# Performance work log

Hardware: AMD Instinct MI355X
Metric: run time of the kernel (lower is better)

## Reference

```python
import jax, jax.numpy as jnp
import numpy as np

B, T, D = 2048, 200, 64
H1, H2 = 80, 40
CONST_MIN = -4294967295.0


def setup_inputs() -> dict:
    key = jax.random.key(0)
    ks = jax.random.split(key, 10)
    q = jax.random.normal(ks[0], (B, D), dtype=jnp.float32)
    k = jax.random.normal(ks[1], (B, T, D), dtype=jnp.float32)
    v = jax.random.normal(ks[2], (B, T, D), dtype=jnp.float32)
    mask = jax.random.randint(ks[3], (B, T), 0, 2, dtype=jnp.int32)
    # MLP params: Dense(80, sigmoid) -> Dense(40, sigmoid) -> Dense(1)
    s1 = 1.0 / np.sqrt(4 * D)
    W1 = jax.random.normal(ks[4], (4 * D, H1), dtype=jnp.float32) * s1
    b1 = jnp.zeros((H1,), dtype=jnp.float32)
    W2 = jax.random.normal(ks[5], (H1, H2), dtype=jnp.float32) * (1.0 / np.sqrt(H1))
    b2 = jnp.zeros((H2,), dtype=jnp.float32)
    Wf = jax.random.normal(ks[6], (H2, 1), dtype=jnp.float32) * (1.0 / np.sqrt(H2))
    bf = jnp.zeros((1,), dtype=jnp.float32)
    return {"q": q, "k": k, "v": v, "mask": mask,
            "W1": W1, "b1": b1, "W2": W2, "b2": b2, "Wf": Wf, "bf": bf}


def reference(q, k, v, mask, W1, b1, W2, b2, Wf, bf):
    # q: [B,D] tiled over T -> [B,T,D]
    qt = jnp.broadcast_to(q[:, None, :], k.shape)
    # per-pair features [B,T,4D]
    info = jnp.concatenate([qt, k, qt - k, qt * k], axis=-1)
    h = jax.nn.sigmoid(jnp.einsum('btf,fh->bth', info, W1) + b1)
    h = jax.nn.sigmoid(jnp.einsum('bth,hg->btg', h, W2) + b2)
    logits = (jnp.einsum('btg,go->bto', h, Wf) + bf)[..., 0]  # [B,T]
    logits = jnp.where(mask == 0, jnp.float32(CONST_MIN), logits)
    w = jax.nn.softmax(logits, axis=-1)  # [B,T]
    out = jnp.einsum('bt,btd->bd', w, v)  # weighted sum of v
    return out
```

## Files before the change

### kernel.cpp

```cpp
#include <hip/hip_runtime.h>
#include <math.h>

#define T_LEN 200

typedef short bf8 __attribute__((ext_vector_type(8)));
typedef float f32x4 __attribute__((ext_vector_type(4)));

__device__ __forceinline__ float sigmoidf_(float x){ return 1.0f/(1.0f+__expf(-x)); }
__device__ __forceinline__ unsigned int pk_bf16(float lo, float hi){
  unsigned int r; asm("v_cvt_pk_bf16_f32 %0, %1, %2":"=v"(r):"v"(lo),"v"(hi)); return r;
}
__device__ __forceinline__ float bfu(short s){
  union{unsigned u; float f;} c; c.u = ((unsigned)(unsigned short)s)<<16; return c.f;
}
union U4B8 { uint4 u; bf8 b; };
__device__ __forceinline__ bf8 pack8(float4 x, float4 y){
  U4B8 r;
  r.u.x = pk_bf16(x.x,x.y); r.u.y = pk_bf16(x.z,x.w);
  r.u.z = pk_bf16(y.x,y.y); r.u.w = pk_bf16(y.z,y.w);
  return r.b;
}
__device__ __forceinline__ bf8 combine8(bf8 fbc, bf8 fd, float4 ql, float4 qh){
  U4B8 r;
  r.u.x = pk_bf16(fmaf(ql.x, bfu(fd[0]), bfu(fbc[0])), fmaf(ql.y, bfu(fd[1]), bfu(fbc[1])));
  r.u.y = pk_bf16(fmaf(ql.z, bfu(fd[2]), bfu(fbc[2])), fmaf(ql.w, bfu(fd[3]), bfu(fbc[3])));
  r.u.z = pk_bf16(fmaf(qh.x, bfu(fd[4]), bfu(fbc[4])), fmaf(qh.y, bfu(fd[5]), bfu(fbc[5])));
  r.u.w = pk_bf16(fmaf(qh.z, bfu(fd[6]), bfu(fbc[6])), fmaf(qh.w, bfu(fd[7]), bfu(fbc[7])));
  return r.b;
}

__global__ void prep_kernel(const float* __restrict__ W1, const float* __restrict__ W2,
                            const float* __restrict__ b2, const float* __restrict__ Wf,
                            float* __restrict__ wsf){
  unsigned short* fb = (unsigned short*)wsf;
  int i = blockIdx.x*256 + threadIdx.x;
  if (i < 15360){
    int fi = i >> 9;
    int lane = (i>>3)&63, e = i&7;
    int ht = fi/6, ks = fi%6;
    int h = ht*16 + (lane&15);
    int f = ks*32 + ((lane>>4)<<3) + e;
    float val;
    if (f < 64)        val = W1[(64+f)*80+h] - W1[(128+f)*80+h];
    else if (f < 128)  val = W1[(128+f)*80+h];
    else               val = W1[(f-128)*80+h] + W1[f*80+h];
    fb[i] = (unsigned short)(pk_bf16(val,val) & 0xffffu);
  }
  if (i < 4608){
    int fi = i >> 9;
    int lane = (i>>3)&63, e = i&7;
    int gt = fi/3, ks = fi%3;
    int g = gt*16 + (lane&15);
    int h = ks*32 + ((lane>>4)<<3) + e;
    float val;
    if (g < 40 && h < 80)       val = W2[h*40+g];
    else if (g < 40 && h == 80) val = b2[g];
    else                        val = 0.f;
    fb[15360+i] = (unsigned short)(pk_bf16(val,val) & 0xffffu);
  }
  if (i < 48){
    wsf[10032 + i] = (i<40) ? Wf[i] : 0.f;
  }
}

__global__ __launch_bounds__(256, 1) void fused_kernel(
    const float* __restrict__ q, const float* __restrict__ k, const float* __restrict__ v,
    const int* __restrict__ mask, const float* __restrict__ b1,
    const float* __restrict__ bf, const float* __restrict__ wsf,
    float* __restrict__ out)
{
  __shared__ unsigned short tl_all[4][224];
  __shared__ __align__(16) unsigned int Hw_all[4][16*52];
  __shared__ float e_all[4][16];
  __shared__ __align__(16) unsigned int w2s[9*64*4];

  const int tid  = threadIdx.x;
  const int lane = tid & 63;
  const int wid  = tid >> 6;
  const int lg = lane>>4, lc = lane&15;
  const long b = (long)blockIdx.x*4 + wid;

  const float* kb = k + b*(T_LEN*64);
  const float* vb = v + b*(T_LEN*64);
  const int*   mb = mask + b*T_LEN;
  const float* qb = q + b*64;
  const unsigned short* fbg = (const unsigned short*)wsf;
  const bf8* A1f = (const bf8*)fbg;
  const uint4* A2u = (const uint4*)(fbg + 15360);
  const float* wfp = wsf + 10032;

  unsigned short* tl = tl_all[wid];
  unsigned int*   Hw = Hw_all[wid];
  float*          e_lds = e_all[wid];

  for (int j = tid; j < 576; j += 256) ((uint4*)w2s)[j] = A2u[j];

  if (lane < 32){
    uint4 z = {0,0,0,0};
    if (!(lane&1)) z.x = 0x00003F80u;
    *(uint4*)(&Hw[(lane>>1)*52 + 40 + (lane&1)*4]) = z;
  }
  __syncthreads();

  float4 qA0 = *(const float4*)(qb + lg*8);
  float4 qA1 = *(const float4*)(qb + lg*8 + 4);
  float4 qB0 = *(const float4*)(qb + 32 + lg*8);
  float4 qB1 = *(const float4*)(qb + 32 + lg*8 + 4);

  bf8 wk[10];
  #pragma unroll
  for (int ht=0; ht<5; ++ht){
    wk[ht*2+0] = combine8(A1f[(ht*6+0)*64+lane], A1f[(ht*6+2)*64+lane], qA0, qA1);
    wk[ht*2+1] = combine8(A1f[(ht*6+1)*64+lane], A1f[(ht*6+3)*64+lane], qB0, qB1);
  }
  float wfv[12];
  #pragma unroll
  for (int gt=0; gt<3; ++gt){
    float4 wv = *(const float4*)(wfp + gt*16 + lg*4);
    wfv[gt*4+0]=wv.x; wfv[gt*4+1]=wv.y; wfv[gt*4+2]=wv.z; wfv[gt*4+3]=wv.w;
  }

  f32x4 qacc[5];
  {
    bf8 fq0 = pack8(qA0,qA1);
    bf8 fq1 = pack8(qB0,qB1);
    #pragma unroll
    for (int ht=0; ht<5; ++ht){
      float4 bv = *(const float4*)(b1 + ht*16 + lg*4);
      qacc[ht][0]=bv.x; qacc[ht][1]=bv.y; qacc[ht][2]=bv.z; qacc[ht][3]=bv.w;
      qacc[ht] = __builtin_amdgcn_mfma_f32_16x16x32_bf16(A1f[(ht*6+4)*64+lane], fq0, qacc[ht],0,0,0);
      qacc[ht] = __builtin_amdgcn_mfma_f32_16x16x32_bf16(A1f[(ht*6+5)*64+lane], fq1, qacc[ht],0,0,0);
    }
  }
  const float bf0 = bf[0];

  int tot = 0;
  unsigned long long ltm = (1ull<<lane) - 1ull;
  #pragma unroll
  for (int c=0;c<4;++c){
    int t = c*64 + lane;
    bool f = (t < T_LEN) && (mb[t] != 0);
    unsigned long long bal = __ballot(f);
    if (f) tl[tot + (int)__popcll(bal & ltm)] = (unsigned short)t;
    tot += (int)__popcll(bal);
  }

  if (tot == 0){
    float accv = 0.f;
    for (int t=0; t<T_LEN; ++t) accv += vb[t*64 + lane];
    out[b*64 + lane] = accv * (1.0f/(float)T_LEN);
    return;
  }

  int tp = tl[min(lc, tot-1)];
  const float* kr = kb + tp*64 + lg*8;
  float4 na0 = *(const float4*)(kr);
  float4 na1 = *(const float4*)(kr+4);
  float4 nb0 = *(const float4*)(kr+32);
  float4 nb1 = *(const float4*)(kr+36);

  float acc_pv0 = 0.f, acc_pv1 = 0.f;
  float se0 = 0.f, se1 = 0.f;
  for (int base = 0; base < tot; base += 16){
    const bool have_next = (base + 16 < tot);
    float vcur[16];
    #pragma unroll
    for (int i=0;i<16;++i){
      int ti = tl[min(base+i, tot-1)];
      vcur[i] = vb[ti*64 + lane];
    }
    bf8 f0 = pack8(na0,na1);
    bf8 f1 = pack8(nb0,nb1);
    if (have_next){
      int tn = tl[min(base+16+lc, tot-1)];
      const float* krn = kb + tn*64 + lg*8;
      na0 = *(const float4*)(krn);
      na1 = *(const float4*)(krn+4);
      nb0 = *(const float4*)(krn+32);
      nb1 = *(const float4*)(krn+36);
    }

    f32x4 acc[5];
    #pragma unroll
    for (int ht=0; ht<5; ++ht) acc[ht] = qacc[ht];
    __builtin_amdgcn_s_setprio(1);
    #pragma unroll
    for (int ht=0; ht<5; ++ht){
      acc[ht] = __builtin_amdgcn_mfma_f32_16x16x32_bf16(wk[ht*2+0], f0, acc[ht],0,0,0);
      acc[ht] = __builtin_amdgcn_mfma_f32_16x16x32_bf16(wk[ht*2+1], f1, acc[ht],0,0,0);
    }
    __builtin_amdgcn_s_setprio(0);

    #pragma unroll
    for (int ht=0; ht<5; ++ht){
      #pragma unroll
      for (int rp=0; rp<2; ++rp)
        Hw[lc*52 + ht*8+lg*2+rp] = pk_bf16(sigmoidf_(acc[ht][2*rp]), sigmoidf_(acc[ht][2*rp+1]));
    }

    bf8 c0[3];
    #pragma unroll
    for (int ks=0; ks<3; ++ks) c0[ks] = *(const bf8*)(Hw + lc*52 + 16*ks + 4*lg);
    f32x4 g0[3];
    #pragma unroll
    for (int gt=0; gt<3; ++gt){ g0[gt][0]=0.f; g0[gt][1]=0.f; g0[gt][2]=0.f; g0[gt][3]=0.f; }
    __builtin_amdgcn_s_setprio(1);
    #pragma unroll
    for (int gt=0; gt<3; ++gt){
      #pragma unroll
      for (int ks=0; ks<3; ++ks){
        bf8 wf2 = *(const bf8*)(w2s + ((gt*3+ks)*64+lane)*4);
        g0[gt] = __builtin_amdgcn_mfma_f32_16x16x32_bf16(wf2, c0[ks], g0[gt],0,0,0);
      }
    }
    __builtin_amdgcn_s_setprio(0);
    float p0=0.f;
    #pragma unroll
    for (int gt=0; gt<3; ++gt){
      #pragma unroll
      for (int r=0;r<4;++r) p0 = fmaf(wfv[gt*4+r], sigmoidf_(g0[gt][r]), p0);
    }
    p0 += __shfl_xor(p0,16); p0 += __shfl_xor(p0,32);
    if (lg == 0) e_lds[lc] = (base+lc < tot) ? __expf(p0 + bf0) : 0.f;

    #pragma unroll
    for (int i=0;i<16;i+=2){
      float ei0 = e_lds[i];
      float ei1 = e_lds[i+1];
      se0 += ei0; se1 += ei1;
      acc_pv0 = fmaf(ei0, vcur[i],   acc_pv0);
      acc_pv1 = fmaf(ei1, vcur[i+1], acc_pv1);
    }
  }

  out[b*64 + lane] = (acc_pv0 + acc_pv1) / (se0 + se1);
}

extern "C" void kernel_launch(void* const* d_in, const int* in_sizes, int n_in,
                              void* d_out, int out_size, void* d_ws, size_t ws_size,
                              hipStream_t stream) {
  const float* q    = (const float*)d_in[0];
  const float* k    = (const float*)d_in[1];
  const float* v    = (const float*)d_in[2];
  const int*   mask = (const int*)d_in[3];
  const float* W1   = (const float*)d_in[4];
  const float* b1   = (const float*)d_in[5];
  const float* W2   = (const float*)d_in[6];
  const float* b2   = (const float*)d_in[7];
  const float* Wf   = (const float*)d_in[8];
  const float* bf   = (const float*)d_in[9];
  float* out = (float*)d_out;
  float* wsf = (float*)d_ws;

  hipLaunchKernelGGL(prep_kernel, dim3(60), dim3(256), 0, stream, W1, W2, b2, Wf, wsf);
  hipLaunchKernelGGL(fused_kernel, dim3(512), dim3(256), 0, stream,
                     q, k, v, mask, b1, bf, wsf, out);
}
```

Measured before the change: 38.28 us.

## Process all timesteps densely with mask bits instead of compacted index list

Drops the LDS compaction of unmasked timestep indices and instead iterates over all 200 timesteps contiguously, applying the mask through ballot bitmasks when computing exp weights. This removes the indirect gather through the index list and the LDS write/read dependency, and gives coalesced, predictable k/v loads. In exchange, it does roughly twice the MFMA and sigmoid work, since about half the steps are masked with random masks.

```diff
diff --git a/kernel.cpp b/kernel.cpp
--- a/kernel.cpp
+++ b/kernel.cpp
@@ -69,7 +69,6 @@
     const float* __restrict__ bf, const float* __restrict__ wsf,
     float* __restrict__ out)
 {
-  __shared__ unsigned short tl_all[4][224];
   __shared__ __align__(16) unsigned int Hw_all[4][16*52];
   __shared__ float e_all[4][16];
   __shared__ __align__(16) unsigned int w2s[9*64*4];
@@ -89,9 +88,8 @@
   const uint4* A2u = (const uint4*)(fbg + 15360);
   const float* wfp = wsf + 10032;
 
-  unsigned short* tl = tl_all[wid];
-  unsigned int*   Hw = Hw_all[wid];
-  float*          e_lds = e_all[wid];
+  unsigned int* Hw = Hw_all[wid];
+  float*        e_lds = e_all[wid];
 
   for (int j = tid; j < 576; j += 256) ((uint4*)w2s)[j] = A2u[j];
 
@@ -101,6 +99,23 @@
     *(uint4*)(&Hw[(lane>>1)*52 + 40 + (lane&1)*4]) = z;
   }
   __syncthreads();
+
+  unsigned long long m0, m1, m2, m3;
+  {
+    bool f;
+    f = (mb[lane] != 0);                              m0 = __ballot(f);
+    f = (mb[64 + lane] != 0);                         m1 = __ballot(f);
+    f = (mb[128 + lane] != 0);                        m2 = __ballot(f);
+    f = (lane < T_LEN - 192) && (mb[192 + lane] != 0); m3 = __ballot(f);
+  }
+  const int tot = (int)(__popcll(m0) + __popcll(m1) + __popcll(m2) + __popcll(m3));
+
+  if (tot == 0){
+    float accv = 0.f;
+    for (int t=0; t<T_LEN; ++t) accv += vb[t*64 + lane];
+    out[b*64 + lane] = accv * (1.0f/(float)T_LEN);
+    return;
+  }
 
   float4 qA0 = *(const float4*)(qb + lg*8);
   float4 qA1 = *(const float4*)(qb + lg*8 + 4);
@@ -134,26 +149,7 @@
   }
   const float bf0 = bf[0];
 
-  int tot = 0;
-  unsigned long long ltm = (1ull<<lane) - 1ull;
-  #pragma unroll
-  for (int c=0;c<4;++c){
-    int t = c*64 + lane;
-    bool f = (t < T_LEN) && (mb[t] != 0);
-    unsigned long long bal = __ballot(f);
-    if (f) tl[tot + (int)__popcll(bal & ltm)] = (unsigned short)t;
-    tot += (int)__popcll(bal);
-  }
-
-  if (tot == 0){
-    float accv = 0.f;
-    for (int t=0; t<T_LEN; ++t) accv += vb[t*64 + lane];
-    out[b*64 + lane] = accv * (1.0f/(float)T_LEN);
-    return;
-  }
-
-  int tp = tl[min(lc, tot-1)];
-  const float* kr = kb + tp*64 + lg*8;
+  const float* kr = kb + lc*64 + lg*8;
   float4 na0 = *(const float4*)(kr);
   float4 na1 = *(const float4*)(kr+4);
   float4 nb0 = *(const float4*)(kr+32);
@@ -161,18 +157,17 @@
 
   float acc_pv0 = 0.f, acc_pv1 = 0.f;
   float se0 = 0.f, se1 = 0.f;
-  for (int base = 0; base < tot; base += 16){
-    const bool have_next = (base + 16 < tot);
+  for (int base = 0; base < T_LEN; base += 16){
     float vcur[16];
     #pragma unroll
     for (int i=0;i<16;++i){
-      int ti = tl[min(base+i, tot-1)];
-      vcur[i] = vb[ti*64 + lane];
+      int row = base + i; row = (row > T_LEN-1) ? (T_LEN-1) : row;
+      vcur[i] = vb[row*64 + lane];
     }
     bf8 f0 = pack8(na0,na1);
     bf8 f1 = pack8(nb0,nb1);
-    if (have_next){
-      int tn = tl[min(base+16+lc, tot-1)];
+    if (base + 16 < T_LEN){
+      int tn = base + 16 + lc; tn = (tn > T_LEN-1) ? (T_LEN-1) : tn;
       const float* krn = kb + tn*64 + lg*8;
       na0 = *(const float4*)(krn);
       na1 = *(const float4*)(krn+4);
@@ -221,7 +216,10 @@
       for (int r=0;r<4;++r) p0 = fmaf(wfv[gt*4+r], sigmoidf_(g0[gt][r]), p0);
     }
     p0 += __shfl_xor(p0,16); p0 += __shfl_xor(p0,32);
-    if (lg == 0) e_lds[lc] = (base+lc < tot) ? __expf(p0 + bf0) : 0.f;
+    unsigned long long mw = (base < 64) ? m0 : (base < 128) ? m1 : (base < 192) ? m2 : m3;
+    unsigned int bit = (unsigned int)(mw >> ((base & 63) + lc)) & 1u;
+    float e_own = bit ? __expf(p0 + bf0) : 0.f;
+    if (lg == 0) e_lds[lc] = e_own;
 
     #pragma unroll
     for (int i=0;i<16;i+=2){
```

Measured after the change: 54.43 us. 42.2% more time.

## Double-buffer V rows into LDS via async global_load_lds prefetch

Applied to the files above, without the earlier changes.

Replaces the per-iteration register gather of 16 V values per lane with asynchronous global-to-LDS loads (16 bytes per lane) into a per-wave double buffer. The loads for the next tile are issued one iteration ahead, and a vmcnt wait guards the current buffer before the softmax-weighted accumulation. The goal is to hide V gather latency behind the MFMA work and cut scattered 4-byte loads. In exchange it adds LDS footprint and relies on precise vmcnt counting, and K prefetch now always issues even on the last tile.

```diff
diff --git a/kernel.cpp b/kernel.cpp
--- a/kernel.cpp
+++ b/kernel.cpp
@@ -27,6 +27,12 @@
   r.u.z = pk_bf16(fmaf(qh.x, bfu(fd[4]), bfu(fbc[4])), fmaf(qh.y, bfu(fd[5]), bfu(fbc[5])));
   r.u.w = pk_bf16(fmaf(qh.z, bfu(fd[6]), bfu(fbc[6])), fmaf(qh.w, bfu(fd[7]), bfu(fbc[7])));
   return r.b;
+}
+__device__ __forceinline__ void gl_lds16(const float* g, float* lds_uniform){
+  __builtin_amdgcn_global_load_lds(
+      (const __attribute__((address_space(1))) unsigned int*)(const void*)g,
+      (__attribute__((address_space(3))) unsigned int*)(void*)lds_uniform,
+      16, 0, 0);
 }
 
 __global__ void prep_kernel(const float* __restrict__ W1, const float* __restrict__ W2,
@@ -72,6 +78,7 @@
   __shared__ unsigned short tl_all[4][224];
   __shared__ __align__(16) unsigned int Hw_all[4][16*52];
   __shared__ float e_all[4][16];
+  __shared__ __align__(16) float vbuf_all[4][2*16*64];
   __shared__ __align__(16) unsigned int w2s[9*64*4];
 
   const int tid  = threadIdx.x;
@@ -92,6 +99,7 @@
   unsigned short* tl = tl_all[wid];
   unsigned int*   Hw = Hw_all[wid];
   float*          e_lds = e_all[wid];
+  float*          vwave = vbuf_all[wid];
 
   for (int j = tid; j < 576; j += 256) ((uint4*)w2s)[j] = A2u[j];
 
@@ -152,26 +160,34 @@
     return;
   }
 
-  int tp = tl[min(lc, tot-1)];
-  const float* kr = kb + tp*64 + lg*8;
-  float4 na0 = *(const float4*)(kr);
-  float4 na1 = *(const float4*)(kr+4);
-  float4 nb0 = *(const float4*)(kr+32);
-  float4 nb1 = *(const float4*)(kr+36);
+  {
+    int tp = tl[min(lc, tot-1)];
+    const float* kr = kb + tp*64 + lg*8;
+  }
+  int tp0 = tl[min(lc, tot-1)];
+  const float* kr0p = kb + tp0*64 + lg*8;
+  float4 na0 = *(const float4*)(kr0p);
+  float4 na1 = *(const float4*)(kr0p+4);
+  float4 nb0 = *(const float4*)(kr0p+32);
+  float4 nb1 = *(const float4*)(kr0p+36);
+  {
+    const int r  = lane >> 4;
+    const int c4 = (lane & 15) << 2;
+    #pragma unroll
+    for (int j=0;j<4;++j){
+      int row = min(4*j + r, tot-1);
+      int trow = tl[row];
+      gl_lds16(vb + trow*64 + c4, vwave + j*256);
+    }
+  }
 
   float acc_pv0 = 0.f, acc_pv1 = 0.f;
   float se0 = 0.f, se1 = 0.f;
-  for (int base = 0; base < tot; base += 16){
-    const bool have_next = (base + 16 < tot);
-    float vcur[16];
-    #pragma unroll
-    for (int i=0;i<16;++i){
-      int ti = tl[min(base+i, tot-1)];
-      vcur[i] = vb[ti*64 + lane];
-    }
+  int cur = 0;
+  for (int base = 0; base < tot; base += 16, cur ^= 1){
     bf8 f0 = pack8(na0,na1);
     bf8 f1 = pack8(nb0,nb1);
-    if (have_next){
+    {
       int tn = tl[min(base+16+lc, tot-1)];
       const float* krn = kb + tn*64 + lg*8;
       na0 = *(const float4*)(krn);
@@ -179,6 +195,17 @@
       nb0 = *(const float4*)(krn+32);
       nb1 = *(const float4*)(krn+36);
     }
+    {
+      float* dstu = vwave + (cur^1)*1024;
+      const int r  = lane >> 4;
+      const int c4 = (lane & 15) << 2;
+      #pragma unroll
+      for (int j=0;j<4;++j){
+        int row = min(base + 16 + 4*j + r, tot-1);
+        int trow = tl[row];
+        gl_lds16(vb + trow*64 + c4, dstu + j*256);
+      }
+    }
 
     f32x4 acc[5];
     #pragma unroll
@@ -223,13 +250,17 @@
     p0 += __shfl_xor(p0,16); p0 += __shfl_xor(p0,32);
     if (lg == 0) e_lds[lc] = (base+lc < tot) ? __expf(p0 + bf0) : 0.f;
 
+    asm volatile("s_waitcnt vmcnt(8)" ::: "memory");
+    __builtin_amdgcn_sched_barrier(0);
+
+    const float* vcb = vwave + cur*1024;
     #pragma unroll
     for (int i=0;i<16;i+=2){
       float ei0 = e_lds[i];
       float ei1 = e_lds[i+1];
       se0 += ei0; se1 += ei1;
-      acc_pv0 = fmaf(ei0, vcur[i],   acc_pv0);
-      acc_pv1 = fmaf(ei1, vcur[i+1], acc_pv1);
+      acc_pv0 = fmaf(ei0, vcb[i*64+lane],     acc_pv0);
+      acc_pv1 = fmaf(ei1, vcb[(i+1)*64+lane], acc_pv1);
     }
   }
 
```

Result: no change. 38.72 us (+1.1%).
